# Performance work log

Measured on AMD Instinct MI355X. Metric: run time of the kernel, lower is better.

The kernel has to match this reference:

```python
import jax, jax.numpy as jnp
import numpy as np

DIM = 64        # feature size per vector
CODES = 512     # codebook size (called d_model in the torch module)
DECAY = 0.99
EPS = 1e-5


def setup_inputs() -> dict:
    key = jax.random.key(0)
    k1, k2 = jax.random.split(key)
    x = jax.random.normal(k1, (64, 64, 64, 64), dtype=jnp.float32)
    embedding = jax.random.normal(k2, (DIM, CODES), dtype=jnp.float32)
    N = jnp.zeros((CODES,), dtype=jnp.float32)
    M = embedding.copy()  # torch module initializes M as embedding.clone()
    return {"x": x, "embedding": embedding, "N": N, "M": M}


def reference(x, embedding, N, M):
    # flatten tokens: [T, DIM]
    flatten = x.reshape(-1, DIM)
    # squared L2 distance to every code: [T, CODES]
    distance = (jnp.sum(flatten * flatten, axis=1, keepdims=True)
                - 2.0 * flatten @ embedding
                + jnp.sum(embedding * embedding, axis=0, keepdims=True))
    max_index = jnp.argmin(distance, axis=1)          # (-distance).max(1) == argmin
    indices = max_index.reshape(x.shape[:-1])
    # gather codes: embedding.T is [CODES, DIM]
    quantize = jnp.take(embedding.T, max_index, axis=0).reshape(x.shape)

    # EMA codebook update (training=True). Avoid materializing onehot:
    # ni = onehot.sum(0); eofx = flatten.T @ onehot  -> segment sums over codes.
    ni = jax.ops.segment_sum(jnp.ones_like(max_index, dtype=jnp.float32),
                             max_index, num_segments=CODES)          # [CODES]
    eofx = jax.ops.segment_sum(flatten, max_index, num_segments=CODES).T  # [DIM, CODES]
    N_new = N * DECAY + (1.0 - DECAY) * ni
    M_new = M * DECAY + (1.0 - DECAY) * eofx
    n = jnp.sum(N_new)
    N_smoothed = (N_new + EPS) / (n + CODES * EPS) * n
    embedding_new = M_new / N_smoothed

    quant_loss = jnp.mean((jax.lax.stop_gradient(x) - quantize) ** 2)
    commitment_loss = jnp.mean((jax.lax.stop_gradient(quantize) - x) ** 2)
    quantize_st = x + jax.lax.stop_gradient(quantize - x)  # straight-through
    return (quantize_st, quant_loss, indices, commitment_loss,
            embedding_new, N_new, M_new)
```

## Files before the change

kernel.cpp:

```cpp
#include <hip/hip_runtime.h>
#include <hip/hip_bf16.h>
#include <math.h>

#define DIM 64
#define CODES 512
#define TOKENS 262144
#define XELEMS 16777216

#define DECAYF 0.99f
#define OMDECAY 0.01f
#define EPSF 1e-5f

#define WS_CNORM 0
#define WS_NI    512
#define WS_EOFX  1024
#define WS_LOSS  33792
#define WS_ET    33808
#define WS_IMG   66576

#define OFF_Q    0
#define OFF_QL   16777216
#define OFF_IDX  16777217
#define OFF_CL   17039361
#define OFF_ENEW 17039362
#define OFF_NNEW 17072130
#define OFF_MNEW 17072642

typedef __attribute__((ext_vector_type(8))) short bf16x8;
typedef __attribute__((ext_vector_type(4))) float f32x4;

static __device__ inline void split_bf(float v, short& hi, short& lo) {
  unsigned int b = __float_as_uint(v);
  unsigned int hb = b & 0xffff0000u;
  float lof = v - __uint_as_float(hb);
  hi = (short)(b >> 16);
  lo = (short)(__float_as_uint(lof) >> 16);
}

__global__ __launch_bounds__(256) void vq_prep(const float* __restrict__ emb,
                                               float* __restrict__ ws) {
  int c = blockIdx.x * 256 + threadIdx.x;
  unsigned short* img = (unsigned short*)(ws + WS_IMG);
  float* eT = ws + WS_ET;
  int cc = c >> 4;
  int n = c & 15;
  float cn = 0.f;
#pragma unroll
  for (int d0 = 0; d0 < DIM; d0 += 4) {
    float v[4];
#pragma unroll
    for (int u = 0; u < 4; ++u) {
      v[u] = emb[(d0 + u) * CODES + c];
      cn = fmaf(v[u], v[u], cn);
    }
    *(float4*)(eT + (size_t)c * DIM + d0) = make_float4(v[0], v[1], v[2], v[3]);
    int kh = d0 >> 5, kk = d0 & 31, qd = kk >> 3, j0 = kk & 7;
    int lane = qd * 16 + n;
    short hi[4], lo[4];
#pragma unroll
    for (int u = 0; u < 4; ++u) split_bf(v[u], hi[u], lo[u]);
    int base = cc * 2048 + kh * 1024 + lane * 8 + j0;
    *(ushort4*)(img + base) =
        make_ushort4((unsigned short)hi[0], (unsigned short)hi[1],
                     (unsigned short)hi[2], (unsigned short)hi[3]);
    *(ushort4*)(img + base + 512) =
        make_ushort4((unsigned short)lo[0], (unsigned short)lo[1],
                     (unsigned short)lo[2], (unsigned short)lo[3]);
  }
  ws[WS_CNORM + c] = cn;
}

__global__ __launch_bounds__(256, 4) void vq_screen(
    const float* __restrict__ x, const float* __restrict__ ws,
    float* __restrict__ loss_sum, float* __restrict__ q_out,
    float* __restrict__ idx_out) {
  __shared__ float cn_l[CODES];

  const float* eT = ws + WS_ET;
  const unsigned short* gimg = (const unsigned short*)(ws + WS_IMG);

  for (int i = threadIdx.x; i < CODES; i += 256) cn_l[i] = ws[WS_CNORM + i];
  __syncthreads();

  const int lane = threadIdx.x & 63;
  const int wave = threadIdx.x >> 6;
  const int n = lane & 15;
  const int quad = lane >> 4;
  const int t0 = blockIdx.x * 256 + wave * 64;

  const float INITP = __uint_as_float((__float_as_uint(1e30f) & 0xFFFFFE00u) | 511u);
  float loss = 0.f;

#pragma unroll 1
  for (int pair = 0; pair < 2; ++pair) {
    bf16x8 ah[2][2], al[2][2];
#pragma unroll
    for (int tile = 0; tile < 2; ++tile) {
      const float* xr =
          x + (size_t)(t0 + (pair * 2 + tile) * 16 + n) * DIM + quad * 8;
#pragma unroll
      for (int kh = 0; kh < 2; ++kh) {
        float4 va = *(const float4*)(xr + kh * 32);
        float4 vb = *(const float4*)(xr + kh * 32 + 4);
        float f[8] = {va.x, va.y, va.z, va.w, vb.x, vb.y, vb.z, vb.w};
#pragma unroll
        for (int j = 0; j < 8; ++j) {
          short hi, lo;
          split_bf(-2.f * f[j], hi, lo);
          ah[tile][kh][j] = hi;
          al[tile][kh][j] = lo;
        }
      }
    }

    float v1[2][4], v2[2][4];
#pragma unroll
    for (int tile = 0; tile < 2; ++tile)
#pragma unroll
      for (int r = 0; r < 4; ++r) {
        v1[tile][r] = INITP;
        v2[tile][r] = INITP;
      }

    bf16x8 Pa0, Pa1, Pa2, Pa3, Pb0, Pb1, Pb2, Pb3;
    {
      const unsigned short* bq = gimg + lane * 8;
      Pa0 = *(const bf16x8*)(bq);
      Pa1 = *(const bf16x8*)(bq + 512);
      Pa2 = *(const bf16x8*)(bq + 1024);
      Pa3 = *(const bf16x8*)(bq + 1536);
    }

    auto ccbody = [&](int cc, const bf16x8& ch0, const bf16x8& cl0,
                      const bf16x8& ch1, const bf16x8& cl1, bf16x8& nh0,
                      bf16x8& nl0, bf16x8& nh1, bf16x8& nl1) {
      const unsigned short* bq = gimg + ((cc + 1) & 31) * 2048 + lane * 8;
      nh0 = *(const bf16x8*)(bq);
      nl0 = *(const bf16x8*)(bq + 512);
      nh1 = *(const bf16x8*)(bq + 1024);
      nl1 = *(const bf16x8*)(bq + 1536);
      float cnv = cn_l[cc * 16 + n];
      unsigned int cid = (unsigned int)(cc * 16 + n);
#pragma unroll
      for (int tile = 0; tile < 2; ++tile) {
        f32x4 acc = {0.f, 0.f, 0.f, 0.f};
        acc = __builtin_amdgcn_mfma_f32_16x16x32_bf16(ah[tile][0], ch0, acc, 0, 0, 0);
        acc = __builtin_amdgcn_mfma_f32_16x16x32_bf16(al[tile][0], ch0, acc, 0, 0, 0);
        acc = __builtin_amdgcn_mfma_f32_16x16x32_bf16(ah[tile][0], cl0, acc, 0, 0, 0);
        acc = __builtin_amdgcn_mfma_f32_16x16x32_bf16(ah[tile][1], ch1, acc, 0, 0, 0);
        acc = __builtin_amdgcn_mfma_f32_16x16x32_bf16(al[tile][1], ch1, acc, 0, 0, 0);
        acc = __builtin_amdgcn_mfma_f32_16x16x32_bf16(ah[tile][1], cl1, acc, 0, 0, 0);
#pragma unroll
        for (int r = 0; r < 4; ++r) {
          float s = acc[r] + cnv;
          float sp = __uint_as_float((__float_as_uint(s) & 0xFFFFFE00u) | cid);
          float o1 = v1[tile][r];
          v2[tile][r] = __builtin_amdgcn_fmed3f(sp, o1, v2[tile][r]);
          v1[tile][r] = fminf(sp, o1);
        }
      }
    };

    for (int cc = 0; cc < 32; cc += 2) {
      ccbody(cc, Pa0, Pa1, Pa2, Pa3, Pb0, Pb1, Pb2, Pb3);
      ccbody(cc + 1, Pb0, Pb1, Pb2, Pb3, Pa0, Pa1, Pa2, Pa3);
    }

#pragma unroll
    for (int m = 1; m < 16; m <<= 1) {
#pragma unroll
      for (int tile = 0; tile < 2; ++tile)
#pragma unroll
        for (int r = 0; r < 4; ++r) {
          float o1 = __shfl_xor(v1[tile][r], m, 16);
          float o2 = __shfl_xor(v2[tile][r], m, 16);
          float a = v1[tile][r];
          v1[tile][r] = fminf(a, o1);
          v2[tile][r] = fminf(fminf(v2[tile][r], o2), fmaxf(a, o1));
        }
    }

#pragma unroll
    for (int tile = 0; tile < 2; ++tile) {
      int tt = pair * 2 + tile;
#pragma unroll
      for (int r = 0; r < 4; ++r) {
        int t = t0 + tt * 16 + quad * 4 + r;
        int c1 = (int)(__float_as_uint(v1[tile][r]) & 511u);
        int c2 = (int)(__float_as_uint(v2[tile][r]) & 511u);
        float4 xv = *(const float4*)(x + (size_t)t * DIM + n * 4);
        float4 e1 = *(const float4*)(eT + (size_t)c1 * DIM + n * 4);
        float4 e2 = *(const float4*)(eT + (size_t)c2 * DIM + n * 4);
        float p1 = xv.x * e1.x;
        p1 = fmaf(xv.y, e1.y, p1);
        p1 = fmaf(xv.z, e1.z, p1);
        p1 = fmaf(xv.w, e1.w, p1);
        float p2 = xv.x * e2.x;
        p2 = fmaf(xv.y, e2.y, p2);
        p2 = fmaf(xv.z, e2.z, p2);
        p2 = fmaf(xv.w, e2.w, p2);
#pragma unroll
        for (int m = 1; m < 16; m <<= 1) {
          p1 += __shfl_xor(p1, m, 16);
          p2 += __shfl_xor(p2, m, 16);
        }
        float d1 = fmaf(-2.f, p1, cn_l[c1]);
        float d2 = fmaf(-2.f, p2, cn_l[c2]);
        bool take2 = (d2 < d1) || (d2 == d1 && c2 < c1);
        int w = take2 ? c2 : c1;
        float4 q = take2 ? e2 : e1;
        *(float4*)(q_out + (size_t)t * DIM + n * 4) = q;
        float u0 = xv.x - q.x, u1 = xv.y - q.y;
        float u2 = xv.z - q.z, u3 = xv.w - q.w;
        loss = fmaf(u0, u0, loss);
        loss = fmaf(u1, u1, loss);
        loss = fmaf(u2, u2, loss);
        loss = fmaf(u3, u3, loss);
        if (n == 0) idx_out[t] = (float)w;
      }
    }
  }

#pragma unroll
  for (int off = 32; off > 0; off >>= 1) loss += __shfl_down(loss, off, 64);
  if (lane == 0) atomicAdd(loss_sum, loss);
}

__global__ __launch_bounds__(1024, 1) void vq_scatter(
    const float* __restrict__ x, const float* __restrict__ idx_out,
    float* __restrict__ ws_acc) {
  __shared__ __align__(16) unsigned char smem[71808];
  float* lds_e = (float*)smem;
  float* lds_n = (float*)(smem + 65664);
  int* win_l = (int*)(smem + 67712);

  const int lane = threadIdx.x & 63;
  const int wave = threadIdx.x >> 6;
  const int n = lane & 15;
  const int quad = lane >> 4;
  const int t0 = blockIdx.x * 1024 + wave * 64;

  {
    float4 z = make_float4(0.f, 0.f, 0.f, 0.f);
    float4* zp = (float4*)smem;
    for (int i = threadIdx.x; i < 67712 / 16; i += 1024) zp[i] = z;
  }
  win_l[threadIdx.x] = (int)idx_out[blockIdx.x * 1024 + threadIdx.x];
  __syncthreads();

  const int rotE = (blockIdx.x & 7) * 2048;
  const int rotN = (blockIdx.x & 7) * 64;

#pragma unroll 1
  for (int kh = 0; kh < 2; ++kh) {
#pragma unroll
    for (int tile = 0; tile < 4; ++tile) {
      int wbi = win_l[wave * 64 + tile * 16 + n];
      if (kh == 0 && quad == 0) atomicAdd(&lds_n[wbi], 1.0f);
      const float* xr =
          x + (size_t)(t0 + tile * 16 + n) * DIM + kh * 32 + quad * 8;
      float4 xa = *(const float4*)(xr);
      float4 xb = *(const float4*)(xr + 4);
      int k0 = quad * 8;
      atomicAdd(&lds_e[(k0 + 0) * 513 + wbi], xa.x);
      atomicAdd(&lds_e[(k0 + 1) * 513 + wbi], xa.y);
      atomicAdd(&lds_e[(k0 + 2) * 513 + wbi], xa.z);
      atomicAdd(&lds_e[(k0 + 3) * 513 + wbi], xa.w);
      atomicAdd(&lds_e[(k0 + 4) * 513 + wbi], xb.x);
      atomicAdd(&lds_e[(k0 + 5) * 513 + wbi], xb.y);
      atomicAdd(&lds_e[(k0 + 6) * 513 + wbi], xb.z);
      atomicAdd(&lds_e[(k0 + 7) * 513 + wbi], xb.w);
    }
    __syncthreads();
    if (kh == 0) {
      for (int ii = threadIdx.x; ii < CODES; ii += 1024) {
        int i = (ii + rotN) & (CODES - 1);
        float v = lds_n[i];
        if (v != 0.f) atomicAdd(&ws_acc[WS_NI + i], v);
      }
    }
    for (int ii = threadIdx.x; ii < 32 * CODES; ii += 1024) {
      int i = (ii + rotE) & (32 * CODES - 1);
      int k = i >> 9, c = i & 511;
      float v = lds_e[k * 513 + c];
      if (v != 0.f) atomicAdd(&ws_acc[WS_EOFX + kh * 32 * CODES + i], v);
      if (kh == 0) lds_e[k * 513 + c] = 0.f;
    }
    if (kh == 0) __syncthreads();
  }
}

__global__ __launch_bounds__(512) void vq_final(const float* __restrict__ Nin,
                                                const float* __restrict__ Min,
                                                const float* __restrict__ ws,
                                                float* __restrict__ out) {
  __shared__ float red[512];
  int c = threadIdx.x;
  int d = blockIdx.x;
  float niv = ws[WS_NI + c];
  float Nn = Nin[c] * DECAYF + OMDECAY * niv;
  red[c] = Nn;
  __syncthreads();
#pragma unroll
  for (int s = 256; s > 0; s >>= 1) {
    if (c < s) red[c] += red[c + s];
    __syncthreads();
  }
  float nsum = red[0];
  float Nsm = (Nn + EPSF) / (nsum + (float)CODES * EPSF) * nsum;
  float m = Min[d * CODES + c] * DECAYF + OMDECAY * ws[WS_EOFX + d * CODES + c];
  out[OFF_MNEW + d * CODES + c] = m;
  out[OFF_ENEW + d * CODES + c] = m / Nsm;
  if (d == 0) {
    out[OFF_NNEW + c] = Nn;
    if (c == 0) {
      float l = ws[WS_LOSS] / (float)XELEMS;
      out[OFF_QL] = l;
      out[OFF_CL] = l;
    }
  }
}

extern "C" void kernel_launch(void* const* d_in, const int* in_sizes, int n_in,
                              void* d_out, int out_size, void* d_ws, size_t ws_size,
                              hipStream_t stream) {
  const float* x = (const float*)d_in[0];
  const float* emb = (const float*)d_in[1];
  const float* Nin = (const float*)d_in[2];
  const float* Min = (const float*)d_in[3];
  float* out = (float*)d_out;
  float* ws = (float*)d_ws;

  hipMemsetAsync(ws + WS_NI, 0, (size_t)(WS_ET - WS_NI) * sizeof(float), stream);

  vq_prep<<<2, 256, 0, stream>>>(emb, ws);

  vq_screen<<<TOKENS / 256, 256, 0, stream>>>(x, ws, ws + WS_LOSS, out + OFF_Q,
                                              out + OFF_IDX);

  vq_scatter<<<TOKENS / 1024, 1024, 0, stream>>>(x, out + OFF_IDX, ws);

  vq_final<<<DIM, 512, 0, stream>>>(Nin, Min, ws, out);
}
```

Baseline: 323.6 us.

## Fuse codebook scatter into screen kernel using direct global atomics

Measured after the change: 1.142 ms. 253% more time.

```diff
diff --git a/kernel.cpp b/kernel.cpp
--- a/kernel.cpp
+++ b/kernel.cpp
@@ -73,7 +73,7 @@
 __global__ __launch_bounds__(256, 4) void vq_screen(
     const float* __restrict__ x, const float* __restrict__ ws,
     float* __restrict__ loss_sum, float* __restrict__ q_out,
-    float* __restrict__ idx_out) {
+    float* __restrict__ idx_out, float* __restrict__ ws_acc) {
   __shared__ float cn_l[CODES];
 
   const float* eT = ws + WS_ET;
@@ -216,7 +216,15 @@
         loss = fmaf(u1, u1, loss);
         loss = fmaf(u2, u2, loss);
         loss = fmaf(u3, u3, loss);
-        if (n == 0) idx_out[t] = (float)w;
+        float* eo = ws_acc + WS_EOFX + (size_t)(n * 4) * CODES + w;
+        atomicAdd(eo, xv.x);
+        atomicAdd(eo + CODES, xv.y);
+        atomicAdd(eo + 2 * CODES, xv.z);
+        atomicAdd(eo + 3 * CODES, xv.w);
+        if (n == 0) {
+          idx_out[t] = (float)w;
+          atomicAdd(&ws_acc[WS_NI + w], 1.0f);
+        }
       }
     }
   }
@@ -224,70 +232,6 @@
 #pragma unroll
   for (int off = 32; off > 0; off >>= 1) loss += __shfl_down(loss, off, 64);
   if (lane == 0) atomicAdd(loss_sum, loss);
-}
-
-__global__ __launch_bounds__(1024, 1) void vq_scatter(
-    const float* __restrict__ x, const float* __restrict__ idx_out,
-    float* __restrict__ ws_acc) {
-  __shared__ __align__(16) unsigned char smem[71808];
-  float* lds_e = (float*)smem;
-  float* lds_n = (float*)(smem + 65664);
-  int* win_l = (int*)(smem + 67712);
-
-  const int lane = threadIdx.x & 63;
-  const int wave = threadIdx.x >> 6;
-  const int n = lane & 15;
-  const int quad = lane >> 4;
-  const int t0 = blockIdx.x * 1024 + wave * 64;
-
-  {
-    float4 z = make_float4(0.f, 0.f, 0.f, 0.f);
-    float4* zp = (float4*)smem;
-    for (int i = threadIdx.x; i < 67712 / 16; i += 1024) zp[i] = z;
-  }
-  win_l[threadIdx.x] = (int)idx_out[blockIdx.x * 1024 + threadIdx.x];
-  __syncthreads();
-
-  const int rotE = (blockIdx.x & 7) * 2048;
-  const int rotN = (blockIdx.x & 7) * 64;
-
-#pragma unroll 1
-  for (int kh = 0; kh < 2; ++kh) {
-#pragma unroll
-    for (int tile = 0; tile < 4; ++tile) {
-      int wbi = win_l[wave * 64 + tile * 16 + n];
-      if (kh == 0 && quad == 0) atomicAdd(&lds_n[wbi], 1.0f);
-      const float* xr =
-          x + (size_t)(t0 + tile * 16 + n) * DIM + kh * 32 + quad * 8;
-      float4 xa = *(const float4*)(xr);
-      float4 xb = *(const float4*)(xr + 4);
-      int k0 = quad * 8;
-      atomicAdd(&lds_e[(k0 + 0) * 513 + wbi], xa.x);
-      atomicAdd(&lds_e[(k0 + 1) * 513 + wbi], xa.y);
-      atomicAdd(&lds_e[(k0 + 2) * 513 + wbi], xa.z);
-      atomicAdd(&lds_e[(k0 + 3) * 513 + wbi], xa.w);
-      atomicAdd(&lds_e[(k0 + 4) * 513 + wbi], xb.x);
-      atomicAdd(&lds_e[(k0 + 5) * 513 + wbi], xb.y);
-      atomicAdd(&lds_e[(k0 + 6) * 513 + wbi], xb.z);
-      atomicAdd(&lds_e[(k0 + 7) * 513 + wbi], xb.w);
-    }
-    __syncthreads();
-    if (kh == 0) {
-      for (int ii = threadIdx.x; ii < CODES; ii += 1024) {
-        int i = (ii + rotN) & (CODES - 1);
-        float v = lds_n[i];
-        if (v != 0.f) atomicAdd(&ws_acc[WS_NI + i], v);
-      }
-    }
-    for (int ii = threadIdx.x; ii < 32 * CODES; ii += 1024) {
-      int i = (ii + rotE) & (32 * CODES - 1);
-      int k = i >> 9, c = i & 511;
-      float v = lds_e[k * 513 + c];
-      if (v != 0.f) atomicAdd(&ws_acc[WS_EOFX + kh * 32 * CODES + i], v);
-      if (kh == 0) lds_e[k * 513 + c] = 0.f;
-    }
-    if (kh == 0) __syncthreads();
-  }
 }
 
 __global__ __launch_bounds__(512) void vq_final(const float* __restrict__ Nin,
@@ -336,9 +280,7 @@
   vq_prep<<<2, 256, 0, stream>>>(emb, ws);
 
   vq_screen<<<TOKENS / 256, 256, 0, stream>>>(x, ws, ws + WS_LOSS, out + OFF_Q,
-                                              out + OFF_IDX);
-
-  vq_scatter<<<TOKENS / 1024, 1024, 0, stream>>>(x, out + OFF_IDX, ws);
+                                              out + OFF_IDX, ws);
 
   vq_final<<<DIM, 512, 0, stream>>>(Nin, Min, ws, out);
 }
```
